# Kernel optimization log

Measured on AMD Instinct MI355X. Metric: run time of the kernel, lower is better.

Reference implementation:

```python
import jax, jax.numpy as jnp
import numpy as np

EMBED_DIM = 768
Q_DIM = 64
V_DIM = 64
WINDOW_SIZE = 3


def setup_inputs() -> dict:
    key = jax.random.key(0)
    ks = jax.random.split(key, 7)
    B, N = 4, 4096
    s = 1.0 / np.sqrt(EMBED_DIM)
    x = jax.random.normal(ks[0], (B, N, EMBED_DIM), dtype=jnp.float32)
    Wq = jax.random.normal(ks[1], (EMBED_DIM, Q_DIM), dtype=jnp.float32) * s
    bq = jax.random.normal(ks[2], (Q_DIM,), dtype=jnp.float32) * 0.01
    Wk = jax.random.normal(ks[3], (EMBED_DIM, Q_DIM), dtype=jnp.float32) * s
    bk = jax.random.normal(ks[4], (Q_DIM,), dtype=jnp.float32) * 0.01
    Wv = jax.random.normal(ks[5], (EMBED_DIM, V_DIM), dtype=jnp.float32) * s
    bv = jax.random.normal(ks[6], (V_DIM,), dtype=jnp.float32) * 0.01
    return {"x": x, "Wq": Wq, "bq": bq, "Wk": Wk, "bk": bk, "Wv": Wv, "bv": bv}


def reference(x, Wq, bq, Wk, bk, Wv, bv):
    # Faithful translation of SliddingWindowAttention.forward, including the
    # original's quirk: diagonal scores are written into columns 0..window_size-1
    # of a full (B, N, N) zero matrix, softmax is taken over ALL N columns
    # (zeros included), and the result is matmul'd with V.
    B, N, _ = x.shape
    Q = x @ Wq + bq  # (B, N, Q_DIM)
    K = x @ Wk + bk  # (B, N, Q_DIM)
    V = x @ Wv + bv  # (B, N, V_DIM)

    half = WINDOW_SIZE // 2
    columns = jnp.zeros((B, N, N), dtype=x.dtype)
    for idx, di in enumerate(range(-half, half + 1)):
        # diagonal offset di: pair row i with column j = i + di (valid rows only)
        rows = np.arange(max(0, -di), N - max(0, di))
        cols_j = rows + di
        c = jnp.einsum('bid,bid->bi', Q[:, rows, :], K[:, cols_j, :])
        columns = columns.at[:, rows, idx].set(c)

    attn = jax.nn.softmax(columns, axis=2)  # (B, N, N)
    return attn @ V  # (B, N, V_DIM)
```

## Files before the change

### kernel.cpp

```cpp
#include <hip/hip_runtime.h>
#include <hip/hip_bf16.h>
#include <math.h>

#define EMBED 768
#define NTOK  4096
#define NB    4
#define ROWS  16384
#define CN    192

typedef __attribute__((ext_vector_type(8))) short bf16x8;
typedef __attribute__((ext_vector_type(8))) unsigned short u16x8;
typedef __attribute__((ext_vector_type(4))) float f32x4;

struct hl16 { unsigned short h, l; };

__device__ inline hl16 split2(float f) {
  hl16 r;
  union { float f; unsigned u; } a; a.f = f;
  unsigned rr = (a.u + 0x7FFFu + ((a.u >> 16) & 1u)) & 0xFFFF0000u;
  r.h = (unsigned short)(rr >> 16);
  union { unsigned u; float f; } hf; hf.u = rr;
  union { float f; unsigned u; } b; b.f = f - hf.f;
  r.l = (unsigned short)((b.u + 0x7FFFu + ((b.u >> 16) & 1u)) >> 16);
  return r;
}

__device__ inline hl16 splitHW(float f) {
  hl16 r;
  __hip_bfloat16 hb = __float2bfloat16(f);
  float hf = __bfloat162float(hb);
  __hip_bfloat16 lb = __float2bfloat16(f - hf);
  r.h = __builtin_bit_cast(unsigned short, hb);
  r.l = __builtin_bit_cast(unsigned short, lb);
  return r;
}

__global__ __launch_bounds__(256) void prep(const float* __restrict__ x,
                                            const float* __restrict__ Wq,
                                            const float* __restrict__ Wk,
                                            const float* __restrict__ Wv,
                                            unsigned short* __restrict__ Wt,
                                            unsigned short* __restrict__ Xt,
                                            float* __restrict__ Vsum) {
  __shared__ float tile[32 * 64];
  const int bid = blockIdx.x;
  const int t   = threadIdx.x;

  if (bid < 6144) {
    const int u   = bid * 4 + (t >> 6);
    const int mt  = u / 24;
    const int ks  = u - mt * 24;
    const int lam = t & 63;
    const int ml  = lam & 15;
    const int q   = lam >> 4;
    const float* src = x + (size_t)(mt * 16 + ml) * EMBED + ks * 32 + q * 8;
    const float4 a0 = *(const float4*)src;
    const float4 a1 = *(const float4*)(src + 4);
    u16x8 hv, lv;
    hl16 s;
    s = splitHW(a0.x); hv[0] = s.h; lv[0] = s.l;
    s = splitHW(a0.y); hv[1] = s.h; lv[1] = s.l;
    s = splitHW(a0.z); hv[2] = s.h; lv[2] = s.l;
    s = splitHW(a0.w); hv[3] = s.h; lv[3] = s.l;
    s = splitHW(a1.x); hv[4] = s.h; lv[4] = s.l;
    s = splitHW(a1.y); hv[5] = s.h; lv[5] = s.l;
    s = splitHW(a1.z); hv[6] = s.h; lv[6] = s.l;
    s = splitHW(a1.w); hv[7] = s.h; lv[7] = s.l;
    unsigned short* dst = Xt + (size_t)(mt * 24 + ks) * 1024 + lam * 8;
    *(u16x8*)dst         = hv;
    *(u16x8*)(dst + 512) = lv;
    return;
  }

  const int b   = bid - 6144;
  const int mat = b / 24;
  const int ks  = b - mat * 24;
  const float* W = (mat == 0) ? Wq : (mat == 1) ? Wk : Wv;

  const float4* src = (const float4*)(W + ks * 2048);
  ((float4*)tile)[t]       = src[t];
  ((float4*)tile)[t + 256] = src[t + 256];
  __syncthreads();

  const int q    = t >> 6;
  const int nloc = t & 63;
  u16x8 hv, lv;
#pragma unroll
  for (int j = 0; j < 8; ++j) {
    hl16 s = split2(tile[(q * 8 + j) * 64 + nloc]);
    hv[j] = s.h; lv[j] = s.l;
  }

  const int n   = mat * 64 + nloc;
  const int nqb = n / 48;
  const int col = n - nqb * 48;
  unsigned short* dst = Wt + (size_t)nqb * 73728 + (size_t)ks * 3072 + q * 384 + col * 8;
  *(u16x8*)dst          = hv;
  *(u16x8*)(dst + 1536) = lv;

  if (b == 0) Vsum[t] = 0.f;
}

__device__ inline void gload_lds16(const unsigned short* g, unsigned short* l) {
  __builtin_amdgcn_global_load_lds(
      (const __attribute__((address_space(1))) unsigned int*)(g),
      (__attribute__((address_space(3))) unsigned int*)(l),
      16, 0, 0);
}

#define MF(A, B, ACC) ACC = __builtin_amdgcn_mfma_f32_16x16x32_bf16(A, B, ACC, 0, 0, 0)

__global__ __launch_bounds__(1024, 4) void qkv_mfma(const unsigned short* __restrict__ Xt,
                                                    const unsigned short* __restrict__ Wtu,
                                                    const float* __restrict__ bq,
                                                    const float* __restrict__ bk,
                                                    const float* __restrict__ bv,
                                                    float* __restrict__ C,
                                                    float* __restrict__ Vsum) {
  extern __shared__ unsigned short lds[];

  const int tid  = threadIdx.x;
  const int lane = tid & 63;
  const int wid  = tid >> 6;
  const int wm   = wid & 7;
  const int kh   = wid >> 3;
  const int nl   = lane & 15;
  const int q    = lane >> 4;
  const int bid  = blockIdx.x;
  const int mc   = (bid & 7) * 8 + (bid >> 5);
  const int nqb  = (bid >> 3) & 3;
  const int nbase = nqb * 48;
  const int r0w  = mc * 256 + wm * 32;
  const int mt0  = mc * 16 + wm * 2;

  {
    const unsigned short* g = Wtu + (size_t)nqb * 73728 + tid * 8;
    unsigned short* l = lds + tid * 8;
#pragma unroll
    for (int i = 0; i < 9; ++i)
      gload_lds16(g + i * 8192, l + i * 8192);
  }

  f32x4 acc00 = {0.f,0.f,0.f,0.f}, acc01 = {0.f,0.f,0.f,0.f}, acc02 = {0.f,0.f,0.f,0.f};
  f32x4 acc10 = {0.f,0.f,0.f,0.f}, acc11 = {0.f,0.f,0.f,0.f}, acc12 = {0.f,0.f,0.f,0.f};

  const bf16x8* XA0 = (const bf16x8*)Xt + ((size_t)mt0 * 24 + kh * 12) * 128 + lane;
  const bf16x8* XA1 = XA0 + 24 * 128;

  bf16x8 ah0 = XA0[0], al0 = XA0[64];
  bf16x8 ah1 = XA1[0], al1 = XA1[64];

  __syncthreads();

  const bf16x8* LB = (const bf16x8*)lds + kh * 12 * 384 + q * 48 + nl;

  for (int s = 0; s < 12; ++s) {
    const int o = s * 384;
    bf16x8 bh0 = LB[o],       bh1 = LB[o + 16],  bh2 = LB[o + 32];
    bf16x8 bl0 = LB[o + 192], bl1 = LB[o + 208], bl2 = LB[o + 224];
    bf16x8 nh0, nl0, nh1, nl1;
    if (s < 11) {
      nh0 = XA0[(s + 1) * 128]; nl0 = XA0[(s + 1) * 128 + 64];
      nh1 = XA1[(s + 1) * 128]; nl1 = XA1[(s + 1) * 128 + 64];
    }
    MF(ah0, bh0, acc00); MF(ah1, bh0, acc10);
    MF(ah0, bh1, acc01); MF(ah1, bh1, acc11);
    MF(ah0, bh2, acc02); MF(ah1, bh2, acc12);
    MF(ah0, bl0, acc00); MF(ah1, bl0, acc10);
    MF(ah0, bl1, acc01); MF(ah1, bl1, acc11);
    MF(ah0, bl2, acc02); MF(ah1, bl2, acc12);
    MF(al0, bh0, acc00); MF(al1, bh0, acc10);
    MF(al0, bh1, acc01); MF(al1, bh1, acc11);
    MF(al0, bh2, acc02); MF(al1, bh2, acc12);
    ah0 = nh0; al0 = nl0; ah1 = nh1; al1 = nl1;
  }

  float* fl = (float*)lds;
  __syncthreads();

#define PST(MI, NT, ACC) do {                                               \
    const int rb = wm * 32 + (MI) * 16 + q * 4;                             \
    const int c  = (NT) * 16 + nl;                                          \
    fl[(rb + 0) * 48 + c] = ACC[0];                                         \
    fl[(rb + 1) * 48 + c] = ACC[1];                                         \
    fl[(rb + 2) * 48 + c] = ACC[2];                                         \
    fl[(rb + 3) * 48 + c] = ACC[3];                                         \
  } while (0)

  if (kh == 1) {
    PST(0, 0, acc00); PST(0, 1, acc01); PST(0, 2, acc02);
    PST(1, 0, acc10); PST(1, 1, acc11); PST(1, 2, acc12);
  }
  __syncthreads();
  if (kh == 1) return;

#define ADDP(MI, NT, ACC) do {                                              \
    const int rb = wm * 32 + (MI) * 16 + q * 4;                             \
    const int c  = (NT) * 16 + nl;                                          \
    ACC[0] += fl[(rb + 0) * 48 + c];                                        \
    ACC[1] += fl[(rb + 1) * 48 + c];                                        \
    ACC[2] += fl[(rb + 2) * 48 + c];                                        \
    ACC[3] += fl[(rb + 3) * 48 + c];                                        \
  } while (0)

  ADDP(0, 0, acc00); ADDP(0, 1, acc01); ADDP(0, 2, acc02);
  ADDP(1, 0, acc10); ADDP(1, 1, acc11); ADDP(1, 2, acc12);

#define EPI(MI, NT, ACC) do {                                               \
    const int col = nbase + (NT) * 16 + nl;                                 \
    const float bias = (col < 64) ? bq[col]                                 \
                     : (col < 128) ? bk[col - 64] : bv[col - 128];          \
    const int row = r0w + (MI) * 16 + q * 4;                                \
    C[(size_t)(row + 0) * CN + col] = ACC[0] + bias;                        \
    C[(size_t)(row + 1) * CN + col] = ACC[1] + bias;                        \
    C[(size_t)(row + 2) * CN + col] = ACC[2] + bias;                        \
    C[(size_t)(row + 3) * CN + col] = ACC[3] + bias;                        \
  } while (0)

  EPI(0, 0, acc00); EPI(0, 1, acc01); EPI(0, 2, acc02);
  EPI(1, 0, acc10); EPI(1, 1, acc11); EPI(1, 2, acc12);

#define VS(NT, A0, A1) do {                                                 \
    const int col = nbase + (NT) * 16 + nl;                                 \
    if (col >= 128) {                                                       \
      float sv = A0[0] + A0[1] + A0[2] + A0[3]                              \
               + A1[0] + A1[1] + A1[2] + A1[3] + 8.f * bv[col - 128];       \
      sv += __shfl_xor(sv, 16, 64);                                         \
      sv += __shfl_xor(sv, 32, 64);                                         \
      if (q == 0) atomicAdd(&Vsum[(r0w >> 12) * 64 + (col - 128)], sv);     \
    }                                                                       \
  } while (0)

  VS(0, acc00, acc10); VS(1, acc01, acc11); VS(2, acc02, acc12);
}

__global__ __launch_bounds__(256) void attn_kernel(const float* __restrict__ C,
                                                   const float* __restrict__ Vsum,
                                                   float* __restrict__ out) {
  const int t    = threadIdx.x;
  const int lane = t & 63;
  const int wave = t >> 6;
  const int r = blockIdx.x * 4 + wave;
  const int b = r >> 12;
  const int i = r & (NTOK - 1);

  const float q  = C[(size_t)r * CN + lane];
  const float kc = C[(size_t)r * CN + 64 + lane];
  float km = 0.f, kp = 0.f;
  if (i > 0)        km = C[(size_t)(r - 1) * CN + 64 + lane];
  if (i < NTOK - 1) kp = C[(size_t)(r + 1) * CN + 64 + lane];

  float p0 = q * km, p1 = q * kc, p2 = q * kp;
#pragma unroll
  for (int off = 32; off > 0; off >>= 1) {
    p0 += __shfl_xor(p0, off, 64);
    p1 += __shfl_xor(p1, off, 64);
    p2 += __shfl_xor(p2, off, 64);
  }

  const float s0 = (i > 0) ? p0 : 0.f;
  const float s1 = p1;
  const float s2 = (i < NTOK - 1) ? p2 : 0.f;
  const float m  = fmaxf(fmaxf(s0, s1), fmaxf(s2, 0.f));
  const float e0 = expf(s0 - m);
  const float e1 = expf(s1 - m);
  const float e2 = expf(s2 - m);
  const float ez = expf(-m);
  const float Z  = e0 + e1 + e2 + (float)(NTOK - 3) * ez;

  const size_t vb = ((size_t)b * NTOK) * CN + 128;
  const float v0 = C[vb + lane];
  const float v1 = C[vb + CN + lane];
  const float v2 = C[vb + 2 * (size_t)CN + lane];
  const float vs = Vsum[b * 64 + lane];

  out[(size_t)r * 64 + lane] =
      (e0 * v0 + e1 * v1 + e2 * v2 + ez * (vs - v0 - v1 - v2)) / Z;
}

extern "C" void kernel_launch(void* const* d_in, const int* in_sizes, int n_in,
                              void* d_out, int out_size, void* d_ws, size_t ws_size,
                              hipStream_t stream) {
  const float* x  = (const float*)d_in[0];
  const float* Wq = (const float*)d_in[1];
  const float* bq = (const float*)d_in[2];
  const float* Wk = (const float*)d_in[3];
  const float* bk = (const float*)d_in[4];
  const float* Wv = (const float*)d_in[5];
  const float* bv = (const float*)d_in[6];
  float* out = (float*)d_out;

  float* C    = (float*)d_ws;
  float* Vsum = C + (size_t)ROWS * CN;
  unsigned short* Wt = (unsigned short*)(Vsum + NB * 64);
  unsigned short* Xt = Wt + 4 * 73728;

  prep<<<6216, 256, 0, stream>>>(x, Wq, Wk, Wv, Wt, Xt, Vsum);
  qkv_mfma<<<256, 1024, 147456, stream>>>(Xt, Wt, bq, bk, bv, C, Vsum);
  attn_kernel<<<ROWS / 4, 256, 0, stream>>>(C, Vsum, out);
}
```

Baseline: 127.5 us.

## Fuse prep, QKV GEMM and attention into one cooperative kernel with grid syncs

Replaces the three launches (prep split, QKV MFMA GEMM, window attention) with a single cooperative kernel of 256 blocks that separates phases with grid-wide syncs. The goal is to remove the launch gaps and tail effects between kernels. Work is redistributed: each block splits a slice of x, the last blocks convert the weights, and the attention phase gives each block 64 rows. The risk is the cost of the grid syncs, lower parallelism in the prep and attention phases, and falling back to three launches if the cooperative launch fails.

```diff
diff --git a/kernel.cpp b/kernel.cpp
--- a/kernel.cpp
+++ b/kernel.cpp
@@ -1,6 +1,9 @@
 #include <hip/hip_runtime.h>
+#include <hip/hip_cooperative_groups.h>
 #include <hip/hip_bf16.h>
 #include <math.h>
+
+namespace cg = cooperative_groups;
 
 #define EMBED 768
 #define NTOK  4096
@@ -33,6 +36,240 @@
   r.h = __builtin_bit_cast(unsigned short, hb);
   r.l = __builtin_bit_cast(unsigned short, lb);
   return r;
+}
+
+__device__ inline void gload_lds16(const unsigned short* g, unsigned short* l) {
+  __builtin_amdgcn_global_load_lds(
+      (const __attribute__((address_space(1))) unsigned int*)(g),
+      (__attribute__((address_space(3))) unsigned int*)(l),
+      16, 0, 0);
+}
+
+#define MF(A, B, ACC) ACC = __builtin_amdgcn_mfma_f32_16x16x32_bf16(A, B, ACC, 0, 0, 0)
+
+__global__ __launch_bounds__(1024, 4) void fused(const float* __restrict__ x,
+                                                 const float* __restrict__ Wq,
+                                                 const float* __restrict__ Wk,
+                                                 const float* __restrict__ Wv,
+                                                 const float* __restrict__ bq,
+                                                 const float* __restrict__ bk,
+                                                 const float* __restrict__ bv,
+                                                 unsigned short* __restrict__ Wt,
+                                                 unsigned short* __restrict__ Xt,
+                                                 float* __restrict__ Vsum,
+                                                 float* __restrict__ C,
+                                                 float* __restrict__ out) {
+  extern __shared__ unsigned short lds[];
+  const int tid  = threadIdx.x;
+  const int bid  = blockIdx.x;
+  const int lane = tid & 63;
+  const int wid  = tid >> 6;
+
+  {
+    const int ml = lane & 15;
+    const int q2 = lane >> 4;
+#pragma unroll
+    for (int i = 0; i < 6; ++i) {
+      const int u  = bid * 96 + wid * 6 + i;
+      const int mt = u / 24;
+      const int ks = u - mt * 24;
+      const float* src = x + (size_t)(mt * 16 + ml) * EMBED + ks * 32 + q2 * 8;
+      const float4 a0 = *(const float4*)src;
+      const float4 a1 = *(const float4*)(src + 4);
+      u16x8 hv, lv;
+      hl16 s;
+      s = splitHW(a0.x); hv[0] = s.h; lv[0] = s.l;
+      s = splitHW(a0.y); hv[1] = s.h; lv[1] = s.l;
+      s = splitHW(a0.z); hv[2] = s.h; lv[2] = s.l;
+      s = splitHW(a0.w); hv[3] = s.h; lv[3] = s.l;
+      s = splitHW(a1.x); hv[4] = s.h; lv[4] = s.l;
+      s = splitHW(a1.y); hv[5] = s.h; lv[5] = s.l;
+      s = splitHW(a1.z); hv[6] = s.h; lv[6] = s.l;
+      s = splitHW(a1.w); hv[7] = s.h; lv[7] = s.l;
+      unsigned short* dst = Xt + (size_t)u * 1024 + lane * 8;
+      *(u16x8*)dst         = hv;
+      *(u16x8*)(dst + 512) = lv;
+    }
+  }
+  if (bid >= 238) {
+    const int task = (bid - 238) * 1024 + tid;
+    if (task < 18432) {
+      const int n    = task / 96;
+      const int ko   = task - n * 96;
+      const int ks   = ko >> 2;
+      const int q2   = ko & 3;
+      const int mat  = n >> 6;
+      const int nloc = n & 63;
+      const float* W = (mat == 0) ? Wq : (mat == 1) ? Wk : Wv;
+      u16x8 hv, lv;
+#pragma unroll
+      for (int j = 0; j < 8; ++j) {
+        hl16 s = split2(W[(size_t)(ks * 32 + q2 * 8 + j) * 64 + nloc]);
+        hv[j] = s.h; lv[j] = s.l;
+      }
+      const int nqb = n / 48;
+      const int col = n - nqb * 48;
+      unsigned short* dst = Wt + (size_t)nqb * 73728 + ks * 3072 + q2 * 384 + col * 8;
+      *(u16x8*)dst          = hv;
+      *(u16x8*)(dst + 1536) = lv;
+    }
+  }
+  if (bid == 0 && tid < NB * 64) Vsum[tid] = 0.f;
+
+  cg::this_grid().sync();
+
+  {
+    const int wm    = wid & 7;
+    const int kh    = wid >> 3;
+    const int nl    = lane & 15;
+    const int q     = lane >> 4;
+    const int mc    = (bid & 7) * 8 + (bid >> 5);
+    const int nqb   = (bid >> 3) & 3;
+    const int nbase = nqb * 48;
+    const int r0w   = mc * 256 + wm * 32;
+    const int mt0   = mc * 16 + wm * 2;
+
+    {
+      const unsigned short* g = Wt + (size_t)nqb * 73728 + tid * 8;
+      unsigned short* l = lds + tid * 8;
+#pragma unroll
+      for (int i = 0; i < 9; ++i)
+        gload_lds16(g + i * 8192, l + i * 8192);
+    }
+
+    f32x4 acc00 = {0.f,0.f,0.f,0.f}, acc01 = {0.f,0.f,0.f,0.f}, acc02 = {0.f,0.f,0.f,0.f};
+    f32x4 acc10 = {0.f,0.f,0.f,0.f}, acc11 = {0.f,0.f,0.f,0.f}, acc12 = {0.f,0.f,0.f,0.f};
+
+    const bf16x8* XA0 = (const bf16x8*)Xt + ((size_t)mt0 * 24 + kh * 12) * 128 + lane;
+    const bf16x8* XA1 = XA0 + 24 * 128;
+
+    bf16x8 ah0 = XA0[0], al0 = XA0[64];
+    bf16x8 ah1 = XA1[0], al1 = XA1[64];
+
+    __syncthreads();
+
+    const bf16x8* LB = (const bf16x8*)lds + kh * 12 * 384 + q * 48 + nl;
+
+    for (int s = 0; s < 12; ++s) {
+      const int o = s * 384;
+      bf16x8 bh0 = LB[o],       bh1 = LB[o + 16],  bh2 = LB[o + 32];
+      bf16x8 bl0 = LB[o + 192], bl1 = LB[o + 208], bl2 = LB[o + 224];
+      bf16x8 nh0, nl0, nh1, nl1;
+      if (s < 11) {
+        nh0 = XA0[(s + 1) * 128]; nl0 = XA0[(s + 1) * 128 + 64];
+        nh1 = XA1[(s + 1) * 128]; nl1 = XA1[(s + 1) * 128 + 64];
+      }
+      MF(ah0, bh0, acc00); MF(ah1, bh0, acc10);
+      MF(ah0, bh1, acc01); MF(ah1, bh1, acc11);
+      MF(ah0, bh2, acc02); MF(ah1, bh2, acc12);
+      MF(ah0, bl0, acc00); MF(ah1, bl0, acc10);
+      MF(ah0, bl1, acc01); MF(ah1, bl1, acc11);
+      MF(ah0, bl2, acc02); MF(ah1, bl2, acc12);
+      MF(al0, bh0, acc00); MF(al1, bh0, acc10);
+      MF(al0, bh1, acc01); MF(al1, bh1, acc11);
+      MF(al0, bh2, acc02); MF(al1, bh2, acc12);
+      ah0 = nh0; al0 = nl0; ah1 = nh1; al1 = nl1;
+    }
+
+    float* fl = (float*)lds;
+    __syncthreads();
+
+#define PST(MI, NT, ACC) do {                                               \
+    const int rb = wm * 32 + (MI) * 16 + q * 4;                             \
+    const int c  = (NT) * 16 + nl;                                          \
+    fl[(rb + 0) * 48 + c] = ACC[0];                                         \
+    fl[(rb + 1) * 48 + c] = ACC[1];                                         \
+    fl[(rb + 2) * 48 + c] = ACC[2];                                         \
+    fl[(rb + 3) * 48 + c] = ACC[3];                                         \
+  } while (0)
+
+    if (kh == 1) {
+      PST(0, 0, acc00); PST(0, 1, acc01); PST(0, 2, acc02);
+      PST(1, 0, acc10); PST(1, 1, acc11); PST(1, 2, acc12);
+    }
+    __syncthreads();
+
+#define ADDP(MI, NT, ACC) do {                                              \
+    const int rb = wm * 32 + (MI) * 16 + q * 4;                             \
+    const int c  = (NT) * 16 + nl;                                          \
+    ACC[0] += fl[(rb + 0) * 48 + c];                                        \
+    ACC[1] += fl[(rb + 1) * 48 + c];                                        \
+    ACC[2] += fl[(rb + 2) * 48 + c];                                        \
+    ACC[3] += fl[(rb + 3) * 48 + c];                                        \
+  } while (0)
+
+#define EPI(MI, NT, ACC) do {                                               \
+    const int col = nbase + (NT) * 16 + nl;                                 \
+    const float bias = (col < 64) ? bq[col]                                 \
+                     : (col < 128) ? bk[col - 64] : bv[col - 128];          \
+    const int row = r0w + (MI) * 16 + q * 4;                                \
+    C[(size_t)(row + 0) * CN + col] = ACC[0] + bias;                        \
+    C[(size_t)(row + 1) * CN + col] = ACC[1] + bias;                        \
+    C[(size_t)(row + 2) * CN + col] = ACC[2] + bias;                        \
+    C[(size_t)(row + 3) * CN + col] = ACC[3] + bias;                        \
+  } while (0)
+
+#define VS(NT, A0, A1) do {                                                 \
+    const int col = nbase + (NT) * 16 + nl;                                 \
+    if (col >= 128) {                                                       \
+      float sv = A0[0] + A0[1] + A0[2] + A0[3]                              \
+               + A1[0] + A1[1] + A1[2] + A1[3] + 8.f * bv[col - 128];       \
+      sv += __shfl_xor(sv, 16, 64);                                         \
+      sv += __shfl_xor(sv, 32, 64);                                         \
+      if (q == 0) atomicAdd(&Vsum[(r0w >> 12) * 64 + (col - 128)], sv);     \
+    }                                                                       \
+  } while (0)
+
+    if (kh == 0) {
+      ADDP(0, 0, acc00); ADDP(0, 1, acc01); ADDP(0, 2, acc02);
+      ADDP(1, 0, acc10); ADDP(1, 1, acc11); ADDP(1, 2, acc12);
+      EPI(0, 0, acc00); EPI(0, 1, acc01); EPI(0, 2, acc02);
+      EPI(1, 0, acc10); EPI(1, 1, acc11); EPI(1, 2, acc12);
+      VS(0, acc00, acc10); VS(1, acc01, acc11); VS(2, acc02, acc12);
+    }
+  }
+
+  cg::this_grid().sync();
+
+  {
+    const int b = (bid * 64) >> 12;
+    const size_t vb = ((size_t)b * NTOK) * CN + 128;
+    const float v0 = C[vb + lane];
+    const float v1 = C[vb + CN + lane];
+    const float v2 = C[vb + 2 * (size_t)CN + lane];
+    const float vs = Vsum[b * 64 + lane];
+#pragma unroll
+    for (int j = 0; j < 4; ++j) {
+      const int r = bid * 64 + wid * 4 + j;
+      const int i = r & (NTOK - 1);
+      const float qv = C[(size_t)r * CN + lane];
+      const float kc = C[(size_t)r * CN + 64 + lane];
+      float km = 0.f, kp = 0.f;
+      if (i > 0)        km = C[(size_t)(r - 1) * CN + 64 + lane];
+      if (i < NTOK - 1) kp = C[(size_t)(r + 1) * CN + 64 + lane];
+
+      float p0 = qv * km, p1 = qv * kc, p2 = qv * kp;
+#pragma unroll
+      for (int off = 32; off > 0; off >>= 1) {
+        p0 += __shfl_xor(p0, off, 64);
+        p1 += __shfl_xor(p1, off, 64);
+        p2 += __shfl_xor(p2, off, 64);
+      }
+
+      const float s0 = (i > 0) ? p0 : 0.f;
+      const float s1 = p1;
+      const float s2 = (i < NTOK - 1) ? p2 : 0.f;
+      const float m  = fmaxf(fmaxf(s0, s1), fmaxf(s2, 0.f));
+      const float e0 = expf(s0 - m);
+      const float e1 = expf(s1 - m);
+      const float e2 = expf(s2 - m);
+      const float ez = expf(-m);
+      const float Z  = e0 + e1 + e2 + (float)(NTOK - 3) * ez;
+
+      out[(size_t)r * 64 + lane] =
+          (e0 * v0 + e1 * v1 + e2 * v2 + ez * (vs - v0 - v1 - v2)) / Z;
+    }
+  }
 }
 
 __global__ __launch_bounds__(256) void prep(const float* __restrict__ x,
@@ -101,15 +338,6 @@
   if (b == 0) Vsum[t] = 0.f;
 }
 
-__device__ inline void gload_lds16(const unsigned short* g, unsigned short* l) {
-  __builtin_amdgcn_global_load_lds(
-      (const __attribute__((address_space(1))) unsigned int*)(g),
-      (__attribute__((address_space(3))) unsigned int*)(l),
-      16, 0, 0);
-}
-
-#define MF(A, B, ACC) ACC = __builtin_amdgcn_mfma_f32_16x16x32_bf16(A, B, ACC, 0, 0, 0)
-
 __global__ __launch_bounds__(1024, 4) void qkv_mfma(const unsigned short* __restrict__ Xt,
                                                     const unsigned short* __restrict__ Wtu,
                                                     const float* __restrict__ bq,
@@ -178,15 +406,6 @@
   float* fl = (float*)lds;
   __syncthreads();
 
-#define PST(MI, NT, ACC) do {                                               \
-    const int rb = wm * 32 + (MI) * 16 + q * 4;                             \
-    const int c  = (NT) * 16 + nl;                                          \
-    fl[(rb + 0) * 48 + c] = ACC[0];                                         \
-    fl[(rb + 1) * 48 + c] = ACC[1];                                         \
-    fl[(rb + 2) * 48 + c] = ACC[2];                                         \
-    fl[(rb + 3) * 48 + c] = ACC[3];                                         \
-  } while (0)
-
   if (kh == 1) {
     PST(0, 0, acc00); PST(0, 1, acc01); PST(0, 2, acc02);
     PST(1, 0, acc10); PST(1, 1, acc11); PST(1, 2, acc12);
@@ -194,42 +413,11 @@
   __syncthreads();
   if (kh == 1) return;
 
-#define ADDP(MI, NT, ACC) do {                                              \
-    const int rb = wm * 32 + (MI) * 16 + q * 4;                             \
-    const int c  = (NT) * 16 + nl;                                          \
-    ACC[0] += fl[(rb + 0) * 48 + c];                                        \
-    ACC[1] += fl[(rb + 1) * 48 + c];                                        \
-    ACC[2] += fl[(rb + 2) * 48 + c];                                        \
-    ACC[3] += fl[(rb + 3) * 48 + c];                                        \
-  } while (0)
-
   ADDP(0, 0, acc00); ADDP(0, 1, acc01); ADDP(0, 2, acc02);
   ADDP(1, 0, acc10); ADDP(1, 1, acc11); ADDP(1, 2, acc12);
 
-#define EPI(MI, NT, ACC) do {                                               \
-    const int col = nbase + (NT) * 16 + nl;                                 \
-    const float bias = (col < 64) ? bq[col]                                 \
-                     : (col < 128) ? bk[col - 64] : bv[col - 128];          \
-    const int row = r0w + (MI) * 16 + q * 4;                                \
-    C[(size_t)(row + 0) * CN + col] = ACC[0] + bias;                        \
-    C[(size_t)(row + 1) * CN + col] = ACC[1] + bias;                        \
-    C[(size_t)(row + 2) * CN + col] = ACC[2] + bias;                        \
-    C[(size_t)(row + 3) * CN + col] = ACC[3] + bias;                        \
-  } while (0)
-
   EPI(0, 0, acc00); EPI(0, 1, acc01); EPI(0, 2, acc02);
   EPI(1, 0, acc10); EPI(1, 1, acc11); EPI(1, 2, acc12);
-
-#define VS(NT, A0, A1) do {                                                 \
-    const int col = nbase + (NT) * 16 + nl;                                 \
-    if (col >= 128) {                                                       \
-      float sv = A0[0] + A0[1] + A0[2] + A0[3]                              \
-               + A1[0] + A1[1] + A1[2] + A1[3] + 8.f * bv[col - 128];       \
-      sv += __shfl_xor(sv, 16, 64);                                         \
-      sv += __shfl_xor(sv, 32, 64);                                         \
-      if (q == 0) atomicAdd(&Vsum[(r0w >> 12) * 64 + (col - 128)], sv);     \
-    }                                                                       \
-  } while (0)
 
   VS(0, acc00, acc10); VS(1, acc01, acc11); VS(2, acc02, acc12);
 }
@@ -295,7 +483,15 @@
   unsigned short* Wt = (unsigned short*)(Vsum + NB * 64);
   unsigned short* Xt = Wt + 4 * 73728;
 
-  prep<<<6216, 256, 0, stream>>>(x, Wq, Wk, Wv, Wt, Xt, Vsum);
-  qkv_mfma<<<256, 1024, 147456, stream>>>(Xt, Wt, bq, bk, bv, C, Vsum);
-  attn_kernel<<<ROWS / 4, 256, 0, stream>>>(C, Vsum, out);
-}
+  void* args[] = {(void*)&x,  (void*)&Wq, (void*)&Wk, (void*)&Wv,
+                  (void*)&bq, (void*)&bk, (void*)&bv,
+                  (void*)&Wt, (void*)&Xt, (void*)&Vsum, (void*)&C, (void*)&out};
+  hipError_t e = hipLaunchCooperativeKernel((const void*)fused, dim3(256),
+                                            dim3(1024), args, 147456, stream);
+  if (e != hipSuccess) {
+    (void)hipGetLastError();
+    prep<<<6216, 256, 0, stream>>>(x, Wq, Wk, Wv, Wt, Xt, Vsum);
+    qkv_mfma<<<256, 1024, 147456, stream>>>(Xt, Wt, bq, bk, bv, C, Vsum);
+    attn_kernel<<<ROWS / 4, 256, 0, stream>>>(C, Vsum, out);
+  }
+}
```

Measured after the change: 222.0 us. +74.2%, slower.
